# Kernel optimization log

Hardware: AMD Instinct MI355X
Metric: run time of the kernel (lower is better)

Reference implementation:

```python
import jax, jax.numpy as jnp
import numpy as np

B, L, D, H = 4, 2048, 1024, 16
d = D // H  # head_dim = 64
EPS = 1e-5
ROPE_BASE = 10000.0


def _rope_tables(seq_len, dim):
    inv_freq = 1.0 / (ROPE_BASE ** (jnp.arange(0, dim, 2, dtype=jnp.float32) / dim))
    t = jnp.arange(seq_len, dtype=jnp.float32)
    freqs = jnp.outer(t, inv_freq)                  # (L, d/2)
    emb = jnp.concatenate([freqs, freqs], axis=-1)  # (L, d)
    return jnp.cos(emb), jnp.sin(emb)


def _rotate_half(x):
    x1, x2 = jnp.split(x, 2, axis=-1)
    return jnp.concatenate([-x2, x1], axis=-1)


def setup_inputs() -> dict:
    key = jax.random.key(0)
    ks = jax.random.split(key, 5)
    x = jax.random.normal(ks[0], (B, L, D), dtype=jnp.float32)
    attn_mask = jnp.ones((B, 1, L, L), dtype=jnp.float32)
    conversion_mask = jax.random.uniform(ks[1], (B, L), dtype=jnp.float32)
    Wqkuv = jax.random.normal(ks[2], (D, 4 * D), dtype=jnp.float32) * (1.0 / np.sqrt(D))
    Wout = jax.random.normal(ks[3], (D, D), dtype=jnp.float32) * (1.0 / np.sqrt(D))
    ln_gamma = jnp.ones((d,), dtype=jnp.float32)
    ln_beta = jnp.zeros((d,), dtype=jnp.float32)
    conv_bias = jax.random.normal(ks[4], (H,), dtype=jnp.float32) * 0.02
    return {"x": x, "attn_mask": attn_mask, "conversion_mask": conversion_mask,
            "Wqkuv": Wqkuv, "Wout": Wout, "ln_gamma": ln_gamma,
            "ln_beta": ln_beta, "conv_bias": conv_bias}


def reference(x, attn_mask, conversion_mask, Wqkuv, Wout, ln_gamma, ln_beta, conv_bias):
    # qkuv projection with SiLU
    qkuv = jax.nn.silu(jnp.einsum('bld,de->ble', x, Wqkuv))  # (B, L, 4D)
    q, k, v, u = jnp.split(qkuv, 4, axis=-1)
    # reshape to (B, H, L, d)
    to_heads = lambda t: t.reshape(B, L, H, d).transpose(0, 2, 1, 3)
    q, k, v, u = map(to_heads, (q, k, v, u))
    # RoPE
    cos, sin = _rope_tables(L, d)            # (L, d)
    cos = cos[None, None]                    # (1,1,L,d)
    sin = sin[None, None]
    q = q * cos + _rotate_half(q) * sin
    k = k * cos + _rotate_half(k) * sin
    # scores + conversion bias + SiLU + multiplicative mask
    scores = jnp.einsum('bhld,bhmd->bhlm', q, k) / jnp.sqrt(jnp.float32(d))
    scores = scores + conversion_mask[:, None, None, :] * conv_bias[None, :, None, None]
    scores = jax.nn.silu(scores)
    scores = scores * attn_mask
    # attend, LayerNorm over head_dim, SiLU-gate with u
    attn_out = jnp.einsum('bhlm,bhmd->bhld', scores, v)
    mu = jnp.mean(attn_out, axis=-1, keepdims=True)
    var = jnp.var(attn_out, axis=-1, keepdims=True)
    attn_out = (attn_out - mu) / jnp.sqrt(var + EPS) * ln_gamma + ln_beta
    attn_out = attn_out * u
    attn_out = attn_out.transpose(0, 2, 1, 3).reshape(B, L, D)
    return jnp.einsum('bld,de->ble', attn_out, Wout)
```

## Files before the change

kernel.cpp:

```cpp
#include <hip/hip_runtime.h>
#include <math.h>
#include <stdint.h>

#define B_ 4
#define L_ 2048
#define D_ 1024
#define H_ 16

typedef __attribute__((ext_vector_type(4))) float f32x4;
typedef __attribute__((ext_vector_type(2))) float f32x2;
typedef __attribute__((ext_vector_type(8))) short s16x8;
typedef __attribute__((ext_vector_type(4))) short s16x4;
typedef __attribute__((ext_vector_type(4))) unsigned short u16x4;
typedef __attribute__((ext_vector_type(4))) unsigned int u32x4;
typedef __attribute__((ext_vector_type(2))) __bf16 bf16x2;

__device__ __forceinline__ unsigned short f2bf(float f) {
  unsigned int u = __float_as_uint(f);
  u += 0x7fffu + ((u >> 16) & 1u);
  return (unsigned short)(u >> 16);
}
__device__ __forceinline__ float b2f(unsigned short s) {
  return __uint_as_float(((unsigned int)s) << 16);
}
__device__ __forceinline__ unsigned int pk2(float a, float b) {
  f32x2 v;
  v[0] = a;
  v[1] = b;
  bf16x2 r = __builtin_convertvector(v, bf16x2);
  return __builtin_bit_cast(unsigned int, r);
}
__device__ __forceinline__ float silu_fast(float v) {
  return v * __builtin_amdgcn_rcpf(1.0f + __expf(-v));
}
__device__ __forceinline__ void gl_lds16(const void* g, void* l) {
  __builtin_amdgcn_global_load_lds(
      (__attribute__((address_space(1))) void*)(uintptr_t)g,
      (__attribute__((address_space(3))) void*)(uint32_t)(uintptr_t)l, 16, 0, 0);
}

__global__ __launch_bounds__(256) void conv_x(const float* __restrict__ x,
                                              unsigned short* __restrict__ xb, int n4) {
  int i = blockIdx.x * 256 + threadIdx.x;
  if (i < n4) {
    f32x4 v = *(const f32x4*)(x + (size_t)i * 4);
    u16x4 o;
#pragma unroll
    for (int j = 0; j < 4; ++j) o[j] = f2bf(v[j]);
    *(u16x4*)(xb + (size_t)i * 4) = o;
  }
}

__global__ __launch_bounds__(256) void trans_w(const float* __restrict__ W,
                                               unsigned short* __restrict__ Wt,
                                               int K, int N) {
  __shared__ float T[64][65];
  const int k0 = blockIdx.y * 64, n0 = blockIdx.x * 64;
  const int tid = threadIdx.x;
#pragma unroll
  for (int i = 0; i < 16; ++i) {
    int e = tid + i * 256;
    int r = e >> 6, c = e & 63;
    T[r][c] = W[(size_t)(k0 + r) * N + n0 + c];
  }
  __syncthreads();
#pragma unroll
  for (int i = 0; i < 16; ++i) {
    int e = tid + i * 256;
    int r = e >> 6, c = e & 63;
    Wt[(size_t)(n0 + r) * K + k0 + c] = f2bf(T[c][r]);
  }
}

__global__ __launch_bounds__(256) void rope_tab(f32x2* __restrict__ tab) {
  int i = blockIdx.x * 256 + threadIdx.x;
  int l = i >> 5, j = i & 31;
  float inv = expf(-(float)j * (9.210340371976184f / 32.0f));
  float ang = (float)l * inv;
  f32x2 cs;
  cs[0] = cosf(ang);
  cs[1] = sinf(ang);
  tab[i] = cs;
}

template <int MODE>
__global__ __launch_bounds__(512) void gemm_bf16(const unsigned short* __restrict__ A,
                                                 const unsigned short* __restrict__ Bt,
                                                 void* __restrict__ Cp,
                                                 int M, int N, int K) {
  alignas(16) __shared__ unsigned short Ash[2][256][64];
  alignas(16) __shared__ unsigned short Bsh[2][256][64];
  const int tid = threadIdx.x;
  const int lane = tid & 63, w = tid >> 6;
  const int quad = lane >> 4, l15 = lane & 15;
  const int wm = w >> 2, wn = w & 3;
  const int nwg = gridDim.x * gridDim.y;
  const int wgid = blockIdx.y * gridDim.x + blockIdx.x;
  const int swz = (wgid & 7) * (nwg >> 3) + (wgid >> 3);
  const int m0 = (swz / gridDim.x) * 256, n0 = (swz % gridDim.x) * 256;

  const int s_sub = lane >> 3;
  const int s_src = (lane & 7) ^ s_sub;

  auto stageA = [&](int k0, int qa, unsigned short(*dst)[64]) {
#pragma unroll
    for (int g = 0; g < 2; ++g) {
      int rb = qa * 64 + g * 128 + w * 8;
      gl_lds16(A + (size_t)(m0 + rb + s_sub) * K + k0 + s_src * 8, &dst[rb][0]);
    }
  };
  auto stageB = [&](int k0, int qb, unsigned short(*dst)[64]) {
#pragma unroll
    for (int g = 0; g < 2; ++g) {
      int rb = qb * 32 + g * 128 + (w >> 2) * 64 + (w & 3) * 8;
      gl_lds16(Bt + (size_t)(n0 + rb + s_sub) * K + k0 + s_src * 8, &dst[rb][0]);
    }
  };

  f32x4 acc[8][4] = {};
  const int NT = K / 64;

  stageA(0, 0, Ash[0]);
  stageB(0, 0, Bsh[0]);
  stageA(0, 1, Ash[0]);
  stageB(0, 1, Bsh[0]);
  asm volatile("s_waitcnt vmcnt(4)" ::: "memory");
  __builtin_amdgcn_s_barrier();
  __builtin_amdgcn_sched_barrier(0);

  for (int t = 0; t < NT; ++t) {
    const int c = t & 1;
#pragma unroll
    for (int p = 0; p < 4; ++p) {
      const int qa = p & 1, qb = p >> 1;
      s16x8 af[4][2], bf[2][2];
#pragma unroll
      for (int i = 0; i < 4; ++i)
#pragma unroll
        for (int ks = 0; ks < 2; ++ks)
          af[i][ks] = *(const s16x8*)&Ash[c][wm * 128 + (qa * 4 + i) * 16 + l15]
                                           [((ks * 4 + quad) ^ (l15 & 7)) * 8];
#pragma unroll
      for (int jn = 0; jn < 2; ++jn)
#pragma unroll
        for (int ks = 0; ks < 2; ++ks)
          bf[jn][ks] = *(const s16x8*)&Bsh[c][wn * 64 + (qb * 2 + jn) * 16 + l15]
                                            [((ks * 4 + quad) ^ (l15 & 7)) * 8];
      if (t + 1 < NT) {
        if (p == 0) stageA((t + 1) * 64, 0, Ash[c ^ 1]);
        if (p == 1) stageB((t + 1) * 64, 0, Bsh[c ^ 1]);
        if (p == 2) stageA((t + 1) * 64, 1, Ash[c ^ 1]);
        if (p == 3) stageB((t + 1) * 64, 1, Bsh[c ^ 1]);
      }
      __builtin_amdgcn_sched_barrier(0);
      __builtin_amdgcn_s_barrier();
      __builtin_amdgcn_sched_barrier(0);
      __builtin_amdgcn_s_setprio(1);
#pragma unroll
      for (int i = 0; i < 4; ++i)
#pragma unroll
        for (int jn = 0; jn < 2; ++jn)
#pragma unroll
          for (int ks = 0; ks < 2; ++ks)
            acc[qa * 4 + i][qb * 2 + jn] = __builtin_amdgcn_mfma_f32_16x16x32_bf16(
                af[i][ks], bf[jn][ks], acc[qa * 4 + i][qb * 2 + jn], 0, 0, 0);
      __builtin_amdgcn_s_setprio(0);
      __builtin_amdgcn_sched_barrier(0);
      if (t + 1 < NT) {
        if (p != 2) asm volatile("s_waitcnt vmcnt(4)" ::: "memory");
      } else {
        if (p == 0) asm volatile("s_waitcnt vmcnt(2)" ::: "memory");
        if (p == 1) asm volatile("s_waitcnt vmcnt(0)" ::: "memory");
      }
      __builtin_amdgcn_s_barrier();
      __builtin_amdgcn_sched_barrier(0);
    }
  }

#pragma unroll
  for (int fm = 0; fm < 8; ++fm)
#pragma unroll
    for (int fn = 0; fn < 4; ++fn)
#pragma unroll
      for (int reg = 0; reg < 4; ++reg) {
        int rg = m0 + wm * 128 + fm * 16 + quad * 4 + reg;
        int cg = n0 + wn * 64 + fn * 16 + l15;
        float v = acc[fm][fn][reg];
        if (MODE == 1) {
          ((unsigned short*)Cp)[(size_t)rg * N + cg] = f2bf(silu_fast(v));
        } else {
          ((float*)Cp)[(size_t)rg * N + cg] = v;
        }
      }
}

template <int MODE>
__global__ __launch_bounds__(256) void gemm128_bf16(const unsigned short* __restrict__ A,
                                                    const unsigned short* __restrict__ Bt,
                                                    void* __restrict__ Cp,
                                                    int M, int N, int K) {
  alignas(16) __shared__ unsigned short As[128][32];
  alignas(16) __shared__ unsigned short Bs[128][32];
  const int tid = threadIdx.x;
  const int lane = tid & 63, w = tid >> 6;
  const int quad = lane >> 4, l15 = lane & 15;
  const int wr = w >> 1, wc = w & 1;
  const int nwg = gridDim.x * gridDim.y;
  const int wgid = blockIdx.y * gridDim.x + blockIdx.x;
  const int swz = (wgid & 7) * (nwg >> 3) + (wgid >> 3);
  const int m0 = (swz / gridDim.x) * 128, n0 = (swz % gridDim.x) * 128;
  const int srow = lane >> 2;
  const int schunk = (lane & 3) ^ ((lane >> 3) & 3);
  const int fcol = (quad ^ ((l15 >> 1) & 3)) * 8;
  f32x4 acc[4][4] = {};
  for (int k0 = 0; k0 < K; k0 += 32) {
    __syncthreads();
#pragma unroll
    for (int i = 0; i < 2; ++i) {
      int r0 = (w * 2 + i) * 16;
      gl_lds16(A + (size_t)(m0 + r0 + srow) * K + k0 + schunk * 8, &As[r0][0]);
      gl_lds16(Bt + (size_t)(n0 + r0 + srow) * K + k0 + schunk * 8, &Bs[r0][0]);
    }
    __syncthreads();
    s16x8 af[4], bf[4];
#pragma unroll
    for (int mi = 0; mi < 4; ++mi) af[mi] = *(const s16x8*)&As[wr * 64 + mi * 16 + l15][fcol];
#pragma unroll
    for (int nj = 0; nj < 4; ++nj) bf[nj] = *(const s16x8*)&Bs[wc * 64 + nj * 16 + l15][fcol];
#pragma unroll
    for (int mi = 0; mi < 4; ++mi)
#pragma unroll
      for (int nj = 0; nj < 4; ++nj)
        acc[mi][nj] = __builtin_amdgcn_mfma_f32_16x16x32_bf16(af[mi], bf[nj], acc[mi][nj], 0, 0, 0);
  }
#pragma unroll
  for (int mi = 0; mi < 4; ++mi)
#pragma unroll
    for (int nj = 0; nj < 4; ++nj)
#pragma unroll
      for (int reg = 0; reg < 4; ++reg) {
        int rg = m0 + wr * 64 + mi * 16 + quad * 4 + reg;
        int cg = n0 + wc * 64 + nj * 16 + l15;
        float v = acc[mi][nj][reg];
        if (MODE == 1) {
          ((unsigned short*)Cp)[(size_t)rg * N + cg] = f2bf(silu_fast(v));
        } else {
          ((float*)Cp)[(size_t)rg * N + cg] = v;
        }
      }
}

__global__ __launch_bounds__(256) void rope_conv(unsigned short* __restrict__ qk,
                                                 unsigned short* __restrict__ vt,
                                                 const f32x2* __restrict__ tab) {
  alignas(16) __shared__ unsigned short Vsh[64][72];
  const int tid = threadIdx.x;
  const int bh = blockIdx.y, b = bh >> 4, h = bh & 15;
  const int l0 = blockIdx.x * 64;
#pragma unroll
  for (int i = 0; i < 2; ++i) {
    int p = tid + i * 256;
    int row = p >> 3, c4 = p & 7;
    int l = l0 + row;
    size_t base = (size_t)(b * L_ + l) * 4096 + h * 64 + c4 * 4;
#pragma unroll
    for (int t = 0; t < 2; ++t) {
      size_t o = base + (size_t)t * 1024;
      u16x4 lo = *(u16x4*)(qk + o);
      u16x4 hi = *(u16x4*)(qk + o + 32);
      u16x4 nlo, nhi;
#pragma unroll
      for (int jj = 0; jj < 4; ++jj) {
        f32x2 cs = tab[l * 32 + c4 * 4 + jj];
        float fl = b2f(lo[jj]), fh = b2f(hi[jj]);
        nlo[jj] = f2bf(fl * cs[0] - fh * cs[1]);
        nhi[jj] = f2bf(fh * cs[0] + fl * cs[1]);
      }
      *(u16x4*)(qk + o) = nlo;
      *(u16x4*)(qk + o + 32) = nhi;
    }
  }
#pragma unroll
  for (int i = 0; i < 2; ++i) {
    int ch = tid + i * 256;
    int row = ch >> 3, c8 = ch & 7;
    *(s16x8*)&Vsh[row][c8 * 8] =
        *(const s16x8*)(qk + (size_t)(b * L_ + l0 + row) * 4096 + 2048 + h * 64 + c8 * 8);
  }
  __syncthreads();
#pragma unroll
  for (int i = 0; i < 2; ++i) {
    int ch = tid + i * 256;
    int drow = ch >> 3, c8 = ch & 7;
    s16x8 o;
#pragma unroll
    for (int jj = 0; jj < 8; ++jj) {
      int pos = c8 * 8 + jj;
      int g = pos >> 5, p = pos & 31;
      int lk = g * 32 + ((p >> 2) & 1) * 16 + ((p >> 3) & 3) * 4 + (p & 3);
      o[jj] = (short)Vsh[lk][drow];
    }
    *(s16x8*)(vt + (size_t)(bh * 64 + drow) * 2048 + l0 + c8 * 8) = o;
  }
}

__global__ __launch_bounds__(256) void attn_mfma(
    const unsigned short* __restrict__ qk, const unsigned short* __restrict__ vt,
    const float* __restrict__ amask, const float* __restrict__ cmask,
    const float* __restrict__ cbias, const float* __restrict__ gamma,
    const float* __restrict__ beta, unsigned short* __restrict__ attng) {
  alignas(16) __shared__ unsigned short Ks[64][64];
  alignas(16) __shared__ unsigned short Vts[64][64];
  const int tid = threadIdx.x;
  const int lane = tid & 63, w = tid >> 6;
  const int quad = lane >> 4, l15 = lane & 15;
  const int bh = blockIdx.y, b = bh >> 4, h = bh & 15;
  const int l0 = blockIdx.x * 128;
  const float cb = cbias[h];
  const int srow = lane >> 3;
  const int schunk = (lane & 7) ^ srow;

  s16x8 qf[2][2];
  const float* abase[2];
#pragma unroll
  for (int qs = 0; qs < 2; ++qs) {
    int qg = l0 + w * 32 + qs * 16 + l15;
#pragma unroll
    for (int s = 0; s < 2; ++s)
      qf[qs][s] = *(const s16x8*)(qk + (size_t)(b * L_ + qg) * 4096 + h * 64 + s * 32 + quad * 8);
    abase[qs] = amask + ((size_t)b * L_ + qg) * L_;
  }
  const float* cbase = cmask + (size_t)b * L_;

  f32x4 oacc[2][4] = {};

  for (int m0 = 0; m0 < L_; m0 += 64) {
    __syncthreads();
#pragma unroll
    for (int i = 0; i < 2; ++i) {
      int r0 = w * 16 + i * 8;
      gl_lds16(qk + (size_t)(b * L_ + m0 + r0 + srow) * 4096 + 1024 + h * 64 + schunk * 8,
               &Ks[r0][0]);
      gl_lds16(vt + (size_t)(bh * 64 + r0 + srow) * 2048 + m0 + schunk * 8, &Vts[r0][0]);
    }
    f32x4 cmcb[4], am4[2][4];
#pragma unroll
    for (int kt = 0; kt < 4; ++kt)
      cmcb[kt] = *(const f32x4*)(cbase + m0 + kt * 16 + quad * 4) * cb;
#pragma unroll
    for (int qs = 0; qs < 2; ++qs)
#pragma unroll
      for (int kt = 0; kt < 4; ++kt)
        am4[qs][kt] = *(const f32x4*)(abase[qs] + m0 + kt * 16 + quad * 4);
    __syncthreads();

    f32x4 sacc[2][4] = {};
#pragma unroll
    for (int s = 0; s < 2; ++s) {
      s16x8 kf[4];
#pragma unroll
      for (int kt = 0; kt < 4; ++kt)
        kf[kt] = *(const s16x8*)&Ks[kt * 16 + l15][((s * 4 + quad) ^ (l15 & 7)) * 8];
      __builtin_amdgcn_s_setprio(1);
#pragma unroll
      for (int qs = 0; qs < 2; ++qs)
#pragma unroll
        for (int kt = 0; kt < 4; ++kt)
          sacc[qs][kt] = __builtin_amdgcn_mfma_f32_16x16x32_bf16(kf[kt], qf[qs][s],
                                                                 sacc[qs][kt], 0, 0, 0);
      __builtin_amdgcn_s_setprio(0);
    }

    s16x8 pf[2][2];
#pragma unroll
    for (int qs = 0; qs < 2; ++qs)
#pragma unroll
      for (int t = 0; t < 2; ++t) {
        u32x4 pw;
#pragma unroll
        for (int half = 0; half < 2; ++half) {
          int kt = 2 * t + half;
          float x[4];
#pragma unroll
          for (int r = 0; r < 4; ++r) {
            float v = fmaf(sacc[qs][kt][r], 0.125f, cmcb[kt][r]);
            v = silu_fast(v);
            x[r] = v * am4[qs][kt][r];
          }
          pw[half * 2 + 0] = pk2(x[0], x[1]);
          pw[half * 2 + 1] = pk2(x[2], x[3]);
        }
        pf[qs][t] = __builtin_bit_cast(s16x8, pw);
      }

#pragma unroll
    for (int dt = 0; dt < 4; ++dt)
#pragma unroll
      for (int t = 0; t < 2; ++t) {
        s16x8 vf = *(const s16x8*)&Vts[dt * 16 + l15][((t * 4 + quad) ^ (l15 & 7)) * 8];
        __builtin_amdgcn_s_setprio(1);
#pragma unroll
        for (int qs = 0; qs < 2; ++qs)
          oacc[qs][dt] = __builtin_amdgcn_mfma_f32_16x16x32_bf16(pf[qs][t], vf,
                                                                 oacc[qs][dt], 0, 0, 0);
        __builtin_amdgcn_s_setprio(0);
      }
  }

#pragma unroll
  for (int qs = 0; qs < 2; ++qs) {
    float sm[4], sq[4];
#pragma unroll
    for (int reg = 0; reg < 4; ++reg) {
      float s1 = 0.f, s2 = 0.f;
#pragma unroll
      for (int dt = 0; dt < 4; ++dt) {
        float v = oacc[qs][dt][reg];
        s1 += v;
        s2 += v * v;
      }
      sm[reg] = s1;
      sq[reg] = s2;
    }
#pragma unroll
    for (int m = 1; m < 16; m <<= 1) {
#pragma unroll
      for (int reg = 0; reg < 4; ++reg) {
        sm[reg] += __shfl_xor(sm[reg], m);
        sq[reg] += __shfl_xor(sq[reg], m);
      }
    }
    float mu[4], rs[4];
#pragma unroll
    for (int reg = 0; reg < 4; ++reg) {
      mu[reg] = sm[reg] * (1.0f / 64.0f);
      float var = sq[reg] * (1.0f / 64.0f) - mu[reg] * mu[reg];
      rs[reg] = rsqrtf(var + 1e-5f);
    }
#pragma unroll
    for (int dt = 0; dt < 4; ++dt) {
      float g = gamma[dt * 16 + l15], be = beta[dt * 16 + l15];
#pragma unroll
      for (int reg = 0; reg < 4; ++reg) {
        int rowg = l0 + w * 32 + qs * 16 + quad * 4 + reg;
        int colg = dt * 16 + l15;
        float v = (oacc[qs][dt][reg] - mu[reg]) * rs[reg] * g + be;
        float u = b2f(qk[(size_t)(b * L_ + rowg) * 4096 + 3072 + h * 64 + colg]);
        attng[(size_t)(b * L_ + rowg) * 1024 + h * 64 + colg] = f2bf(v * u);
      }
    }
  }
}

extern "C" void kernel_launch(void* const* d_in, const int* in_sizes, int n_in,
                              void* d_out, int out_size, void* d_ws, size_t ws_size,
                              hipStream_t stream) {
  const float* x = (const float*)d_in[0];
  const float* amask = (const float*)d_in[1];
  const float* cmask = (const float*)d_in[2];
  const float* Wqkuv = (const float*)d_in[3];
  const float* Wout = (const float*)d_in[4];
  const float* gamma = (const float*)d_in[5];
  const float* beta = (const float*)d_in[6];
  const float* cbias = (const float*)d_in[7];
  float* out = (float*)d_out;

  char* ws = (char*)d_ws;
  unsigned short* qkuv_bf = (unsigned short*)ws;
  unsigned short* vt = (unsigned short*)(ws + ((size_t)64 << 20));
  unsigned short* xbf = (unsigned short*)(ws + ((size_t)80 << 20));
  unsigned short* Wt = (unsigned short*)(ws + ((size_t)96 << 20));
  unsigned short* Wot = (unsigned short*)(ws + ((size_t)104 << 20));
  unsigned short* attng = (unsigned short*)(ws + ((size_t)106 << 20));
  f32x2* tab = (f32x2*)(ws + ((size_t)122 << 20));

  conv_x<<<8192, 256, 0, stream>>>(x, xbf, (B_ * L_ * D_) / 4);
  trans_w<<<dim3(4096 / 64, 1024 / 64), 256, 0, stream>>>(Wqkuv, Wt, 1024, 4096);
  trans_w<<<dim3(1024 / 64, 1024 / 64), 256, 0, stream>>>(Wout, Wot, 1024, 1024);
  rope_tab<<<(L_ * 32) / 256, 256, 0, stream>>>(tab);

  gemm_bf16<1><<<dim3(4096 / 256, 8192 / 256), 512, 0, stream>>>(xbf, Wt, qkuv_bf,
                                                                 B_ * L_, 4 * D_, D_);
  rope_conv<<<dim3(L_ / 64, B_ * H_), 256, 0, stream>>>(qkuv_bf, vt, tab);
  attn_mfma<<<dim3(L_ / 128, B_ * H_), 256, 0, stream>>>(qkuv_bf, vt, amask, cmask, cbias,
                                                         gamma, beta, attng);
  gemm128_bf16<0><<<dim3(1024 / 128, 8192 / 128), 256, 0, stream>>>(attng, Wot, out,
                                                                    B_ * L_, D_, D_);
}
```

Baseline: 452.7 us.

## Fuse RoPE into QKUV GEMM epilogue and merge prep kernels into one launch

The four setup kernels (x conversion, two weight transposes, RoPE table) become a single block-indexed prep launch, which removes launch overhead. RoPE is now applied to the q and k columns in the epilogue of the QKUV GEMM while the accumulators are still in registers. This removes the separate read-modify-write pass over q and k in bf16 that the old rope_conv kernel did, and also drops one bf16 rounding before the rotation. The cost is extra table loads and a branch in the GEMM epilogue, and the epilogue relies on each wave's 64 columns lining up with one head's half-split pairing.

```diff
diff --git a/kernel.cpp b/kernel.cpp
--- a/kernel.cpp
+++ b/kernel.cpp
@@ -39,54 +39,65 @@
       (__attribute__((address_space(3))) void*)(uint32_t)(uintptr_t)l, 16, 0, 0);
 }
 
-__global__ __launch_bounds__(256) void conv_x(const float* __restrict__ x,
-                                              unsigned short* __restrict__ xb, int n4) {
-  int i = blockIdx.x * 256 + threadIdx.x;
-  if (i < n4) {
+__global__ __launch_bounds__(256) void prep(const float* __restrict__ x,
+                                            unsigned short* __restrict__ xb,
+                                            const float* __restrict__ Wqkuv,
+                                            unsigned short* __restrict__ Wt,
+                                            const float* __restrict__ Wout,
+                                            unsigned short* __restrict__ Wot,
+                                            f32x2* __restrict__ tab) {
+  const int bid = blockIdx.x;
+  const int tid = threadIdx.x;
+  if (bid < 8192) {
+    int i = bid * 256 + tid;
     f32x4 v = *(const f32x4*)(x + (size_t)i * 4);
     u16x4 o;
 #pragma unroll
     for (int j = 0; j < 4; ++j) o[j] = f2bf(v[j]);
     *(u16x4*)(xb + (size_t)i * 4) = o;
-  }
-}
-
-__global__ __launch_bounds__(256) void trans_w(const float* __restrict__ W,
-                                               unsigned short* __restrict__ Wt,
-                                               int K, int N) {
-  __shared__ float T[64][65];
-  const int k0 = blockIdx.y * 64, n0 = blockIdx.x * 64;
-  const int tid = threadIdx.x;
-#pragma unroll
-  for (int i = 0; i < 16; ++i) {
-    int e = tid + i * 256;
-    int r = e >> 6, c = e & 63;
-    T[r][c] = W[(size_t)(k0 + r) * N + n0 + c];
-  }
-  __syncthreads();
-#pragma unroll
-  for (int i = 0; i < 16; ++i) {
-    int e = tid + i * 256;
-    int r = e >> 6, c = e & 63;
-    Wt[(size_t)(n0 + r) * K + k0 + c] = f2bf(T[c][r]);
-  }
-}
-
-__global__ __launch_bounds__(256) void rope_tab(f32x2* __restrict__ tab) {
-  int i = blockIdx.x * 256 + threadIdx.x;
-  int l = i >> 5, j = i & 31;
-  float inv = expf(-(float)j * (9.210340371976184f / 32.0f));
-  float ang = (float)l * inv;
-  f32x2 cs;
-  cs[0] = cosf(ang);
-  cs[1] = sinf(ang);
-  tab[i] = cs;
+  } else if (bid < 9472) {
+    __shared__ float T[64][65];
+    const float* W;
+    unsigned short* Wd;
+    int K, N, bx, by;
+    if (bid < 9216) {
+      int e = bid - 8192;
+      W = Wqkuv; Wd = Wt; K = 1024; N = 4096; bx = e & 63; by = e >> 6;
+    } else {
+      int e = bid - 9216;
+      W = Wout; Wd = Wot; K = 1024; N = 1024; bx = e & 15; by = e >> 4;
+    }
+    const int k0 = by * 64, n0 = bx * 64;
+#pragma unroll
+    for (int i = 0; i < 16; ++i) {
+      int e = tid + i * 256;
+      int r = e >> 6, c = e & 63;
+      T[r][c] = W[(size_t)(k0 + r) * N + n0 + c];
+    }
+    __syncthreads();
+#pragma unroll
+    for (int i = 0; i < 16; ++i) {
+      int e = tid + i * 256;
+      int r = e >> 6, c = e & 63;
+      Wd[(size_t)(n0 + r) * K + k0 + c] = f2bf(T[c][r]);
+    }
+  } else {
+    int i = (bid - 9472) * 256 + tid;
+    int l = i >> 5, j = i & 31;
+    float inv = expf(-(float)j * (9.210340371976184f / 32.0f));
+    float ang = (float)l * inv;
+    f32x2 cs;
+    cs[0] = cosf(ang);
+    cs[1] = sinf(ang);
+    tab[i] = cs;
+  }
 }
 
 template <int MODE>
 __global__ __launch_bounds__(512) void gemm_bf16(const unsigned short* __restrict__ A,
                                                  const unsigned short* __restrict__ Bt,
                                                  void* __restrict__ Cp,
+                                                 const f32x2* __restrict__ tab,
                                                  int M, int N, int K) {
   alignas(16) __shared__ unsigned short Ash[2][256][64];
   alignas(16) __shared__ unsigned short Bsh[2][256][64];
@@ -177,21 +188,42 @@
     }
   }
 
-#pragma unroll
-  for (int fm = 0; fm < 8; ++fm)
-#pragma unroll
-    for (int fn = 0; fn < 4; ++fn)
+  if (MODE == 1 && n0 < 2048) {
+#pragma unroll
+    for (int fm = 0; fm < 8; ++fm)
 #pragma unroll
       for (int reg = 0; reg < 4; ++reg) {
         int rg = m0 + wm * 128 + fm * 16 + quad * 4 + reg;
-        int cg = n0 + wn * 64 + fn * 16 + l15;
-        float v = acc[fm][fn][reg];
-        if (MODE == 1) {
-          ((unsigned short*)Cp)[(size_t)rg * N + cg] = f2bf(silu_fast(v));
-        } else {
-          ((float*)Cp)[(size_t)rg * N + cg] = v;
+        int l = rg & (L_ - 1);
+        f32x2 cs0 = tab[l * 32 + l15];
+        f32x2 cs1 = tab[l * 32 + 16 + l15];
+        float v0 = silu_fast(acc[fm][0][reg]);
+        float v1 = silu_fast(acc[fm][1][reg]);
+        float v2 = silu_fast(acc[fm][2][reg]);
+        float v3 = silu_fast(acc[fm][3][reg]);
+        unsigned short* rowp = (unsigned short*)Cp + (size_t)rg * N + n0 + wn * 64 + l15;
+        rowp[0] = f2bf(v0 * cs0[0] - v2 * cs0[1]);
+        rowp[16] = f2bf(v1 * cs1[0] - v3 * cs1[1]);
+        rowp[32] = f2bf(v2 * cs0[0] + v0 * cs0[1]);
+        rowp[48] = f2bf(v3 * cs1[0] + v1 * cs1[1]);
+      }
+  } else {
+#pragma unroll
+    for (int fm = 0; fm < 8; ++fm)
+#pragma unroll
+      for (int fn = 0; fn < 4; ++fn)
+#pragma unroll
+        for (int reg = 0; reg < 4; ++reg) {
+          int rg = m0 + wm * 128 + fm * 16 + quad * 4 + reg;
+          int cg = n0 + wn * 64 + fn * 16 + l15;
+          float v = acc[fm][fn][reg];
+          if (MODE == 1) {
+            ((unsigned short*)Cp)[(size_t)rg * N + cg] = f2bf(silu_fast(v));
+          } else {
+            ((float*)Cp)[(size_t)rg * N + cg] = v;
+          }
         }
-      }
+  }
 }
 
 template <int MODE>
@@ -250,36 +282,12 @@
       }
 }
 
-__global__ __launch_bounds__(256) void rope_conv(unsigned short* __restrict__ qk,
-                                                 unsigned short* __restrict__ vt,
-                                                 const f32x2* __restrict__ tab) {
+__global__ __launch_bounds__(256) void vt_build(const unsigned short* __restrict__ qk,
+                                                unsigned short* __restrict__ vt) {
   alignas(16) __shared__ unsigned short Vsh[64][72];
   const int tid = threadIdx.x;
   const int bh = blockIdx.y, b = bh >> 4, h = bh & 15;
   const int l0 = blockIdx.x * 64;
-#pragma unroll
-  for (int i = 0; i < 2; ++i) {
-    int p = tid + i * 256;
-    int row = p >> 3, c4 = p & 7;
-    int l = l0 + row;
-    size_t base = (size_t)(b * L_ + l) * 4096 + h * 64 + c4 * 4;
-#pragma unroll
-    for (int t = 0; t < 2; ++t) {
-      size_t o = base + (size_t)t * 1024;
-      u16x4 lo = *(u16x4*)(qk + o);
-      u16x4 hi = *(u16x4*)(qk + o + 32);
-      u16x4 nlo, nhi;
-#pragma unroll
-      for (int jj = 0; jj < 4; ++jj) {
-        f32x2 cs = tab[l * 32 + c4 * 4 + jj];
-        float fl = b2f(lo[jj]), fh = b2f(hi[jj]);
-        nlo[jj] = f2bf(fl * cs[0] - fh * cs[1]);
-        nhi[jj] = f2bf(fh * cs[0] + fl * cs[1]);
-      }
-      *(u16x4*)(qk + o) = nlo;
-      *(u16x4*)(qk + o + 32) = nhi;
-    }
-  }
 #pragma unroll
   for (int i = 0; i < 2; ++i) {
     int ch = tid + i * 256;
@@ -474,14 +482,11 @@
   unsigned short* attng = (unsigned short*)(ws + ((size_t)106 << 20));
   f32x2* tab = (f32x2*)(ws + ((size_t)122 << 20));
 
-  conv_x<<<8192, 256, 0, stream>>>(x, xbf, (B_ * L_ * D_) / 4);
-  trans_w<<<dim3(4096 / 64, 1024 / 64), 256, 0, stream>>>(Wqkuv, Wt, 1024, 4096);
-  trans_w<<<dim3(1024 / 64, 1024 / 64), 256, 0, stream>>>(Wout, Wot, 1024, 1024);
-  rope_tab<<<(L_ * 32) / 256, 256, 0, stream>>>(tab);
-
-  gemm_bf16<1><<<dim3(4096 / 256, 8192 / 256), 512, 0, stream>>>(xbf, Wt, qkuv_bf,
+  prep<<<9728, 256, 0, stream>>>(x, xbf, Wqkuv, Wt, Wout, Wot, tab);
+
+  gemm_bf16<1><<<dim3(4096 / 256, 8192 / 256), 512, 0, stream>>>(xbf, Wt, qkuv_bf, tab,
                                                                  B_ * L_, 4 * D_, D_);
-  rope_conv<<<dim3(L_ / 64, B_ * H_), 256, 0, stream>>>(qkuv_bf, vt, tab);
+  vt_build<<<dim3(L_ / 64, B_ * H_), 256, 0, stream>>>(qkuv_bf, vt);
   attn_mfma<<<dim3(L_ / 128, B_ * H_), 256, 0, stream>>>(qkuv_bf, vt, amask, cmask, cbias,
                                                          gamma, beta, attng);
   gemm128_bf16<0><<<dim3(1024 / 128, 8192 / 128), 256, 0, stream>>>(attng, Wot, out,
```

Result: no change. 445.1 us (-1.7%).
